# Kernel tuning notes

Hardware: AMD Instinct MI355X
Metric: run time of the kernel (lower is better)

## Reference

```python
import jax, jax.numpy as jnp
import numpy as np

X_DIM = 362
N_EXPERTS = 3
HIDDEN = [1024, 2048, 2048, 1024]  # layer widths; final layer maps back to X_DIM


def _init_params(key):
    dims = [X_DIM] + HIDDEN + [X_DIM]
    params = {}
    for li in range(len(dims) - 1):
        fan_in = dims[li]
        kW, kb, key = jax.random.split(key, 3)
        bound = 1.0 / np.sqrt(fan_in)
        # stacked over experts: [E, in, out]
        params[f"W{li}"] = jax.random.uniform(kW, (N_EXPERTS, dims[li], dims[li + 1]), jnp.float32, -bound, bound)
        params[f"b{li}"] = jax.random.uniform(kb, (N_EXPERTS, dims[li + 1]), jnp.float32, -bound, bound)
    return params


def setup_inputs() -> dict:
    key = jax.random.key(0)
    kx, kn, ka, kp = jax.random.split(key, 4)
    B = 8192
    inp = {
        "batch_x": jax.random.normal(kx, (B, X_DIM), jnp.float32),
        "batch_next": jax.random.normal(kn, (B, X_DIM), jnp.float32),
        "batch_a": jax.random.randint(ka, (B,), 0, N_EXPERTS, jnp.int64),
    }
    inp.update(_init_params(kp))
    return inp


def _experts_forward(x, W0, b0, W1, b1, W2, b2, W3, b3, W4, b4):
    # Run every expert on the full batch (dense grouped GEMMs), then select.
    # h: [E, B, d]
    h = jax.nn.relu(jnp.einsum("bi,eio->ebo", x, W0) + b0[:, None, :])
    h = jax.nn.relu(jnp.einsum("ebi,eio->ebo", h, W1) + b1[:, None, :])
    h = jax.nn.relu(jnp.einsum("ebi,eio->ebo", h, W2) + b2[:, None, :])
    h = jax.nn.relu(jnp.einsum("ebi,eio->ebo", h, W3) + b3[:, None, :])
    return jnp.einsum("ebi,eio->ebo", h, W4) + b4[:, None, :]  # [E, B, X_DIM]


def reference(batch_x, batch_next, batch_a, W0, b0, W1, b1, W2, b2, W3, b3, W4, b4):
    preds = _experts_forward(batch_x, W0, b0, W1, b1, W2, b2, W3, b3, W4, b4)
    # route: pick each sample's prediction from its action's expert
    pred_next = preds[batch_a, jnp.arange(batch_x.shape[0])]  # [B, X_DIM]
    return jnp.mean((pred_next - batch_next) ** 2)
```

## Files before the change

kernel.cpp:

```cpp
#include <hip/hip_runtime.h>
#include <hip/hip_bf16.h>

#define B_SZ   8192
#define XD     362
#define NEXP   3
#define NTILES 70
#define MP     (NTILES*128)

typedef __bf16 bf16x8 __attribute__((ext_vector_type(8)));
typedef float  f32x4  __attribute__((ext_vector_type(4)));

__device__ __forceinline__ unsigned short f2bf(float f) {
    unsigned u = __float_as_uint(f);
    u += 0x7fffu + ((u >> 16) & 1u);
    return (unsigned short)(u >> 16);
}

__global__ __launch_bounds__(1024) void k_route(const int* __restrict__ a,
                                                int* __restrict__ hdr,
                                                int* __restrict__ row_of) {
    __shared__ int sc[3][1024];
    int tid = threadIdx.x;
    int ev[8];
    int c0 = 0, c1 = 0, c2 = 0;
#pragma unroll
    for (int j = 0; j < 8; ++j) {
        int e = a[tid * 8 + j];
        ev[j] = e;
        c0 += (e == 0); c1 += (e == 1); c2 += (e == 2);
    }
    sc[0][tid] = c0; sc[1][tid] = c1; sc[2][tid] = c2;
    __syncthreads();
    for (int off = 1; off < 1024; off <<= 1) {
        int v0 = (tid >= off) ? sc[0][tid - off] : 0;
        int v1 = (tid >= off) ? sc[1][tid - off] : 0;
        int v2 = (tid >= off) ? sc[2][tid - off] : 0;
        __syncthreads();
        sc[0][tid] += v0; sc[1][tid] += v1; sc[2][tid] += v2;
        __syncthreads();
    }
    int tot0 = sc[0][1023], tot1 = sc[1][1023], tot2 = sc[2][1023];
    int t0 = ((tot0 + 255) >> 8) << 1;
    int t1 = ((tot1 + 255) >> 8) << 1;
    int t2 = ((tot2 + 255) >> 8) << 1;
    int seg0 = 0, seg1 = t0 * 128, seg2 = (t0 + t1) * 128;
    int nt = t0 + t1 + t2;
    int b0 = seg0 + sc[0][tid] - c0;
    int b1 = seg1 + sc[1][tid] - c1;
    int b2 = seg2 + sc[2][tid] - c2;
#pragma unroll
    for (int j = 0; j < 8; ++j) {
        int e = ev[j];
        int pos = (e == 0) ? b0++ : (e == 1) ? b1++ : b2++;
        row_of[pos] = tid * 8 + j;
    }
    if (tid == 0) {
        hdr[0] = tot0; hdr[1] = tot1; hdr[2] = tot2;
        hdr[6] = seg0; hdr[7] = seg1; hdr[8] = seg2;
        hdr[12] = nt;
        hdr[13] = nt / 2 - 1;
        hdr[16] = 0;
    }
    if (tid < NTILES)
        hdr[32 + tid] = (tid < t0) ? 0 : (tid < t0 + t1) ? 1 : (tid < nt) ? 2 : -1;
    for (int r = tid; r < MP; r += 1024) {
        int pad;
        if (r < seg1)           pad = (r - seg0) >= tot0;
        else if (r < seg2)      pad = (r - seg1) >= tot1;
        else if (r < nt * 128)  pad = (r - seg2) >= tot2;
        else                    pad = 1;
        if (pad) row_of[r] = -1;
    }
}

__global__ void k_gather(const float* __restrict__ x, const int* __restrict__ row_of,
                         unsigned short* __restrict__ xg) {
    int r = blockIdx.x;
    int c = threadIdx.x;
    int orig = row_of[r];
    float v = (orig >= 0 && c < XD) ? x[(size_t)orig * XD + c] : 0.f;
    xg[(size_t)r * 384 + c] = f2bf(v);
}

__global__ void k_transpose(const float* __restrict__ W, unsigned short* __restrict__ Wt,
                            int K, int N, int Kp, int Np) {
    __shared__ float t[64][33];
    int e  = blockIdx.z;
    int kb = blockIdx.x * 64, nb = blockIdx.y * 32;
    const float* We = W + (size_t)e * K * N;
    unsigned short* Wte = Wt + (size_t)e * Np * Kp;
    int tx = threadIdx.x, ty = threadIdx.y;
#pragma unroll
    for (int j = 0; j < 8; ++j) {
        int k = kb + ty + j * 8, n = nb + tx;
        t[ty + j * 8][tx] = (k < K && n < N) ? We[(size_t)k * N + n] : 0.f;
    }
    __syncthreads();
#pragma unroll
    for (int j = 0; j < 4; ++j) {
        int n = ty + j * 8;
        unsigned int lo = f2bf(t[2 * tx][n]);
        unsigned int hi = f2bf(t[2 * tx + 1][n]);
        *(unsigned int*)&Wte[(size_t)(nb + n) * Kp + kb + 2 * tx] = lo | (hi << 16);
    }
}

template <int TM, int TN, int WAVES, bool FINAL, bool TAIL, bool SKIPLAST>
__global__ __launch_bounds__(WAVES * 64) void k_gemm(
    const unsigned short* __restrict__ A, int lda,
    const unsigned short* __restrict__ Bt, int K, int Np,
    const float* __restrict__ bias, int nvalid,
    unsigned short* __restrict__ C, int ldc,
    const int* __restrict__ hdr,
    const float* __restrict__ nextv, const int* __restrict__ row_of,
    float* __restrict__ accum)
{
    __shared__ unsigned short As[2][TM * 64];
    __shared__ unsigned short Bs[2][TN * 64];
    __shared__ float red[WAVES];

    constexpr int WGN = TN / 64;
    constexpr int LA  = TM / (WAVES * 8);
    constexpr int LB  = TN / (WAVES * 8);

    int mt128;
    if constexpr (TAIL) {
        mt128 = hdr[13] * 2 + blockIdx.y;
    } else {
        if (SKIPLAST && (int)blockIdx.y >= hdr[13] && TM == 256) return;
        mt128 = blockIdx.y * (TM / 128);
    }
    int e = hdr[32 + mt128];
    if (e < 0) return;
    int row0 = mt128 * 128;
    int n0   = blockIdx.x * TN;

    int tid  = threadIdx.x;
    int wid  = tid >> 6, lane = tid & 63;
    int quad = lane >> 4, l15 = lane & 15;
    int sw   = l15 & 7;
    int wm = (wid / WGN) * 64, wn = (wid % WGN) * 64;

    const unsigned short* Ag = A  + (size_t)row0 * lda;
    const unsigned short* Bg = Bt + (size_t)e * Np * K + (size_t)n0 * K;
    const float* be = bias + (size_t)e * nvalid;

    int srow = lane >> 3;
    int scol = ((lane & 7) ^ srow) * 8;

    f32x4 acc[4][4];
#pragma unroll
    for (int i = 0; i < 4; ++i)
#pragma unroll
        for (int j = 0; j < 4; ++j)
            acc[i][j] = (f32x4){0.f, 0.f, 0.f, 0.f};

#define STAGE(K0, P)                                                              \
    {                                                                             \
        _Pragma("unroll")                                                         \
        for (int ii = 0; ii < LA; ++ii) {                                         \
            int rbase = wid * (TM / WAVES) + ii * 8;                              \
            const unsigned short* gp = Ag + (size_t)(rbase + srow) * lda + (K0) + scol; \
            __builtin_amdgcn_global_load_lds(                                     \
                (const __attribute__((address_space(1))) void*)gp,                \
                (__attribute__((address_space(3))) void*)(As[P] + rbase * 64), 16, 0, 0); \
        }                                                                         \
        _Pragma("unroll")                                                         \
        for (int ii = 0; ii < LB; ++ii) {                                         \
            int rbase = wid * (TN / WAVES) + ii * 8;                              \
            const unsigned short* gp = Bg + (size_t)(rbase + srow) * K + (K0) + scol;   \
            __builtin_amdgcn_global_load_lds(                                     \
                (const __attribute__((address_space(1))) void*)gp,                \
                (__attribute__((address_space(3))) void*)(Bs[P] + rbase * 64), 16, 0, 0); \
        }                                                                         \
    }

#define COMPUTE(P)                                                                \
    {                                                                             \
        _Pragma("unroll")                                                         \
        for (int kh = 0; kh < 2; ++kh) {                                          \
            bf16x8 af[4], bfr[4];                                                 \
            _Pragma("unroll")                                                     \
            for (int f = 0; f < 4; ++f) {                                         \
                int row = wm + f * 16 + l15;                                      \
                af[f] = *(const bf16x8*)(As[P] + row * 64 + (((kh * 4 + quad) ^ sw) << 3)); \
            }                                                                     \
            _Pragma("unroll")                                                     \
            for (int f = 0; f < 4; ++f) {                                         \
                int row = wn + f * 16 + l15;                                      \
                bfr[f] = *(const bf16x8*)(Bs[P] + row * 64 + (((kh * 4 + quad) ^ sw) << 3)); \
            }                                                                     \
            _Pragma("unroll")                                                     \
            for (int fm = 0; fm < 4; ++fm)                                        \
                _Pragma("unroll")                                                 \
                for (int fn = 0; fn < 4; ++fn)                                    \
                    acc[fm][fn] = __builtin_amdgcn_mfma_f32_16x16x32_bf16(        \
                        af[fm], bfr[fn], acc[fm][fn], 0, 0, 0);                   \
        }                                                                         \
    }

    STAGE(0, 0);
    __syncthreads();
    for (int k0 = 0; k0 < K; k0 += 128) {
        if (k0 + 64 < K) STAGE(k0 + 64, 1);
        COMPUTE(0);
        __syncthreads();
        if (k0 + 128 < K) STAGE(k0 + 128, 0);
        COMPUTE(1);
        __syncthreads();
    }
#undef STAGE
#undef COMPUTE

    if constexpr (!FINAL) {
#pragma unroll
        for (int fn = 0; fn < 4; ++fn) {
            int n = n0 + wn + fn * 16 + l15;
            float bv = be[n];
#pragma unroll
            for (int fm = 0; fm < 4; ++fm) {
#pragma unroll
                for (int i = 0; i < 4; ++i) {
                    int r = row0 + wm + fm * 16 + quad * 4 + i;
                    float v = acc[fm][fn][i] + bv;
                    v = v > 0.f ? v : 0.f;
                    C[(size_t)r * ldc + n] = f2bf(v);
                }
            }
        }
    } else {
        float local = 0.f;
#pragma unroll
        for (int fm = 0; fm < 4; ++fm) {
#pragma unroll
            for (int i = 0; i < 4; ++i) {
                int r = row0 + wm + fm * 16 + quad * 4 + i;
                int orig = row_of[r];
                if (orig >= 0) {
                    const float* nrow = nextv + (size_t)orig * XD;
#pragma unroll
                    for (int fn = 0; fn < 4; ++fn) {
                        int n = n0 + wn + fn * 16 + l15;
                        if (n < XD) {
                            float v = acc[fm][fn][i] + be[n];
                            float d = v - nrow[n];
                            local += d * d;
                        }
                    }
                }
            }
        }
        for (int off = 32; off > 0; off >>= 1)
            local += __shfl_down(local, off, 64);
        if (lane == 0) red[wid] = local;
        __syncthreads();
        if (tid == 0) {
            float s = 0.f;
#pragma unroll
            for (int w = 0; w < WAVES; ++w) s += red[w];
            atomicAdd(accum, s);
        }
    }
}

__global__ void k_final(const int* hdr, float* out) {
    if (blockIdx.x == 0 && threadIdx.x == 0) {
        float s = ((const float*)hdr)[16];
        out[0] = s / (float)(B_SZ * XD);
    }
}

extern "C" void kernel_launch(void* const* d_in, const int* in_sizes, int n_in,
                              void* d_out, int out_size, void* d_ws, size_t ws_size,
                              hipStream_t stream) {
    const float* x     = (const float*)d_in[0];
    const float* nextv = (const float*)d_in[1];
    const int*   a     = (const int*)d_in[2];
    const float* W0 = (const float*)d_in[3],  *b0 = (const float*)d_in[4];
    const float* W1 = (const float*)d_in[5],  *b1 = (const float*)d_in[6];
    const float* W2 = (const float*)d_in[7],  *b2 = (const float*)d_in[8];
    const float* W3 = (const float*)d_in[9],  *b3 = (const float*)d_in[10];
    const float* W4 = (const float*)d_in[11], *b4 = (const float*)d_in[12];

    int* hdr    = (int*)d_ws;
    int* row_of = hdr + 128;
    unsigned short* xg = (unsigned short*)(row_of + MP);
    unsigned short* hA = xg + (size_t)MP * 384;
    unsigned short* hB = hA + (size_t)MP * 2048;
    unsigned short* Wt = hB + (size_t)MP * 2048;
    float* accum = (float*)(hdr + 16);

    k_route <<<1, 1024, 0, stream>>>(a, hdr, row_of);
    k_gather<<<MP, 384, 0, stream>>>(x, row_of, xg);

    k_transpose<<<dim3(6, 32, 3), dim3(32, 8), 0, stream>>>(W0, Wt, XD, 1024, 384, 1024);
    k_gemm<128, 128, 4, false, false, false><<<dim3(8, NTILES), 256, 0, stream>>>(
        xg, 384, Wt, 384, 1024, b0, 1024, hA, 1024, hdr, nullptr, nullptr, nullptr);

    k_transpose<<<dim3(16, 64, 3), dim3(32, 8), 0, stream>>>(W1, Wt, 1024, 2048, 1024, 2048);
    k_gemm<256, 256, 16, false, false, true><<<dim3(8, NTILES / 2), 1024, 0, stream>>>(
        hA, 1024, Wt, 1024, 2048, b1, 2048, hB, 2048, hdr, nullptr, nullptr, nullptr);
    k_gemm<128, 128, 4, false, true, false><<<dim3(16, 2), 256, 0, stream>>>(
        hA, 1024, Wt, 1024, 2048, b1, 2048, hB, 2048, hdr, nullptr, nullptr, nullptr);

    k_transpose<<<dim3(32, 64, 3), dim3(32, 8), 0, stream>>>(W2, Wt, 2048, 2048, 2048, 2048);
    k_gemm<256, 256, 16, false, false, true><<<dim3(8, NTILES / 2), 1024, 0, stream>>>(
        hB, 2048, Wt, 2048, 2048, b2, 2048, hA, 2048, hdr, nullptr, nullptr, nullptr);
    k_gemm<128, 128, 4, false, true, false><<<dim3(16, 2), 256, 0, stream>>>(
        hB, 2048, Wt, 2048, 2048, b2, 2048, hA, 2048, hdr, nullptr, nullptr, nullptr);

    k_transpose<<<dim3(32, 32, 3), dim3(32, 8), 0, stream>>>(W3, Wt, 2048, 1024, 2048, 1024);
    k_gemm<256, 256, 16, false, false, true><<<dim3(4, NTILES / 2), 1024, 0, stream>>>(
        hA, 2048, Wt, 2048, 1024, b3, 1024, hB, 1024, hdr, nullptr, nullptr, nullptr);
    k_gemm<128, 128, 4, false, true, false><<<dim3(8, 2), 256, 0, stream>>>(
        hA, 2048, Wt, 2048, 1024, b3, 1024, hB, 1024, hdr, nullptr, nullptr, nullptr);

    k_transpose<<<dim3(16, 12, 3), dim3(32, 8), 0, stream>>>(W4, Wt, 1024, XD, 1024, 384);
    k_gemm<128, 128, 4, true, false, false><<<dim3(3, NTILES), 256, 0, stream>>>(
        hB, 1024, Wt, 1024, 384, b4, XD, nullptr, 0, hdr, nextv, row_of, accum);

    k_final<<<1, 64, 0, stream>>>(hdr, (float*)d_out);
}
```

Before: 523.9 us.

## Add 8-wave 256x256 GEMM with global-to-LDS loads and interleaved pipeline

```diff
diff --git a/kernel.cpp b/kernel.cpp
--- a/kernel.cpp
+++ b/kernel.cpp
@@ -263,6 +263,174 @@
     }
 }
 
+template <bool SKIPLAST>
+__global__ __launch_bounds__(512, 2) void k_gemm8(
+    const unsigned short* __restrict__ A, int lda,
+    const unsigned short* __restrict__ Bt, int K, int Np,
+    const float* __restrict__ bias,
+    unsigned short* __restrict__ C, int ldc,
+    const int* __restrict__ hdr)
+{
+    __shared__ unsigned short As[2][256 * 64];
+    __shared__ unsigned short Bs[2][256 * 64];
+
+    if (SKIPLAST && (int)blockIdx.y >= hdr[13]) return;
+    int mt128 = blockIdx.y * 2;
+    int e = hdr[32 + mt128];
+    if (e < 0) return;
+    int row0 = mt128 * 128;
+    int n0   = blockIdx.x * 256;
+
+    int tid  = threadIdx.x;
+    int wid  = tid >> 6, lane = tid & 63;
+    int quad = lane >> 4, l15 = lane & 15;
+    int wmi  = wid >> 2, wni = wid & 3;
+    int srow = lane >> 3;
+    int scol = ((lane & 7) ^ srow) * 8;
+
+    const unsigned short* Ag = A  + (size_t)row0 * lda;
+    const unsigned short* Bg = Bt + (size_t)e * Np * K + (size_t)n0 * K;
+
+    f32x4 acc[8][4];
+#pragma unroll
+    for (int i = 0; i < 8; ++i)
+#pragma unroll
+        for (int j = 0; j < 4; ++j)
+            acc[i][j] = (f32x4){0.f, 0.f, 0.f, 0.f};
+
+    bf16x8 bfr[4][2];
+    bf16x8 af[2][2];
+
+#define STG(GP, LD, DS, H, KC)                                                    \
+    {                                                                             \
+        _Pragma("unroll")                                                         \
+        for (int ii = 0; ii < 2; ++ii) {                                          \
+            int rbase = (H) * 128 + wid * 16 + ii * 8;                            \
+            const unsigned short* gp = (GP) + (size_t)(rbase + srow) * (LD) + (KC) + scol; \
+            __builtin_amdgcn_global_load_lds(                                     \
+                (const __attribute__((address_space(1))) void*)gp,                \
+                (__attribute__((address_space(3))) void*)((DS) + rbase * 64), 16, 0, 0); \
+        }                                                                         \
+    }
+
+#define LDB8(BUF)                                                                 \
+    {                                                                             \
+        _Pragma("unroll")                                                         \
+        for (int nf = 0; nf < 4; ++nf) {                                          \
+            int row = wni * 64 + nf * 16 + l15;                                   \
+            _Pragma("unroll")                                                     \
+            for (int ks = 0; ks < 2; ++ks)                                        \
+                bfr[nf][ks] = *(const bf16x8*)(Bs[BUF] + row * 64 +               \
+                                               (((ks * 4 + quad) ^ (l15 & 7)) << 3)); \
+        }                                                                         \
+    }
+
+#define LDAQ(BUF, Q)                                                              \
+    {                                                                             \
+        _Pragma("unroll")                                                         \
+        for (int mf = 0; mf < 2; ++mf) {                                          \
+            int row = wmi * 128 + ((Q) * 2 + mf) * 16 + l15;                      \
+            _Pragma("unroll")                                                     \
+            for (int ks = 0; ks < 2; ++ks)                                        \
+                af[mf][ks] = *(const bf16x8*)(As[BUF] + row * 64 +                \
+                                              (((ks * 4 + quad) ^ (l15 & 7)) << 3)); \
+        }                                                                         \
+    }
+
+#define MM16(Q)                                                                   \
+    {                                                                             \
+        _Pragma("unroll")                                                         \
+        for (int mf = 0; mf < 2; ++mf)                                            \
+            _Pragma("unroll")                                                     \
+            for (int nf = 0; nf < 4; ++nf)                                        \
+                _Pragma("unroll")                                                 \
+                for (int ks = 0; ks < 2; ++ks)                                    \
+                    acc[(Q) * 2 + mf][nf] = __builtin_amdgcn_mfma_f32_16x16x32_bf16( \
+                        af[mf][ks], bfr[nf][ks], acc[(Q) * 2 + mf][nf], 0, 0, 0); \
+    }
+
+#define BAR    __builtin_amdgcn_s_barrier()
+#define FENCE  asm volatile("" ::: "memory")
+#define LGKM0  { asm volatile("s_waitcnt lgkmcnt(0)" ::: "memory"); __builtin_amdgcn_sched_barrier(0); }
+#define VM4    asm volatile("s_waitcnt vmcnt(4)" ::: "memory")
+#define VM0    asm volatile("s_waitcnt vmcnt(0)" ::: "memory")
+#define PRIO1  __builtin_amdgcn_s_setprio(1)
+#define PRIO0  __builtin_amdgcn_s_setprio(0)
+
+    STG(Ag, lda, As[0], 0, 0);  STG(Ag, lda, As[0], 1, 0);
+    STG(Bg, K,   Bs[0], 0, 0);  STG(Bg, K,   Bs[0], 1, 0);
+    STG(Bg, K,   Bs[1], 0, 64); STG(Bg, K,   Bs[1], 1, 64);
+    VM4; BAR; FENCE;
+
+    int NT = K >> 6;
+    for (int t = 0; t + 4 <= NT; t += 2) {
+        int kc1 = (t + 1) << 6, kc2 = (t + 2) << 6, kc3 = (t + 3) << 6;
+        LDB8(0); LDAQ(0, 0); STG(Ag, lda, As[1], 0, kc1);
+        BAR; LGKM0; PRIO1; MM16(0); PRIO0; BAR; FENCE;
+        LDAQ(0, 1); STG(Ag, lda, As[1], 1, kc1);
+        BAR; LGKM0; PRIO1; MM16(1); PRIO0; BAR; FENCE;
+        LDAQ(0, 2); STG(Bg, K, Bs[0], 0, kc2);
+        BAR; LGKM0; PRIO1; MM16(2); PRIO0; BAR; FENCE;
+        LDAQ(0, 3); STG(Bg, K, Bs[0], 1, kc2);
+        BAR; LGKM0; PRIO1; MM16(3); PRIO0; VM4; BAR; FENCE;
+        LDB8(1); LDAQ(1, 0); STG(Ag, lda, As[0], 0, kc2);
+        BAR; LGKM0; PRIO1; MM16(0); PRIO0; BAR; FENCE;
+        LDAQ(1, 1); STG(Ag, lda, As[0], 1, kc2);
+        BAR; LGKM0; PRIO1; MM16(1); PRIO0; BAR; FENCE;
+        LDAQ(1, 2); STG(Bg, K, Bs[1], 0, kc3);
+        BAR; LGKM0; PRIO1; MM16(2); PRIO0; BAR; FENCE;
+        LDAQ(1, 3); STG(Bg, K, Bs[1], 1, kc3);
+        BAR; LGKM0; PRIO1; MM16(3); PRIO0; VM4; BAR; FENCE;
+    }
+    {
+        int kc1 = (NT - 1) << 6;
+        LDB8(0); LDAQ(0, 0); STG(Ag, lda, As[1], 0, kc1);
+        BAR; LGKM0; PRIO1; MM16(0); PRIO0; BAR; FENCE;
+        LDAQ(0, 1); STG(Ag, lda, As[1], 1, kc1);
+        BAR; LGKM0; PRIO1; MM16(1); PRIO0; BAR; FENCE;
+        LDAQ(0, 2);
+        BAR; LGKM0; PRIO1; MM16(2); PRIO0; BAR; FENCE;
+        LDAQ(0, 3);
+        BAR; LGKM0; PRIO1; MM16(3); PRIO0; VM0; BAR; FENCE;
+        LDB8(1); LDAQ(1, 0);
+        BAR; LGKM0; PRIO1; MM16(0); PRIO0; BAR; FENCE;
+        LDAQ(1, 1);
+        BAR; LGKM0; PRIO1; MM16(1); PRIO0; BAR; FENCE;
+        LDAQ(1, 2);
+        BAR; LGKM0; PRIO1; MM16(2); PRIO0; BAR; FENCE;
+        LDAQ(1, 3);
+        BAR; LGKM0; PRIO1; MM16(3); PRIO0;
+    }
+#undef STG
+#undef LDB8
+#undef LDAQ
+#undef MM16
+#undef BAR
+#undef FENCE
+#undef LGKM0
+#undef VM4
+#undef VM0
+#undef PRIO1
+#undef PRIO0
+
+    const float* be = bias + (size_t)e * Np;
+#pragma unroll
+    for (int nf = 0; nf < 4; ++nf) {
+        int n = n0 + wni * 64 + nf * 16 + l15;
+        float bv = be[n];
+#pragma unroll
+        for (int m8 = 0; m8 < 8; ++m8) {
+#pragma unroll
+            for (int i = 0; i < 4; ++i) {
+                int r = row0 + wmi * 128 + m8 * 16 + quad * 4 + i;
+                float v = acc[m8][nf][i] + bv;
+                v = v > 0.f ? v : 0.f;
+                C[(size_t)r * ldc + n] = f2bf(v);
+            }
+        }
+    }
+}
+
 __global__ void k_final(const int* hdr, float* out) {
     if (blockIdx.x == 0 && threadIdx.x == 0) {
         float s = ((const float*)hdr)[16];
@@ -298,21 +466,19 @@
         xg, 384, Wt, 384, 1024, b0, 1024, hA, 1024, hdr, nullptr, nullptr, nullptr);
 
     k_transpose<<<dim3(16, 64, 3), dim3(32, 8), 0, stream>>>(W1, Wt, 1024, 2048, 1024, 2048);
-    k_gemm<256, 256, 16, false, false, true><<<dim3(8, NTILES / 2), 1024, 0, stream>>>(
-        hA, 1024, Wt, 1024, 2048, b1, 2048, hB, 2048, hdr, nullptr, nullptr, nullptr);
+    k_gemm8<true><<<dim3(8, NTILES / 2), 512, 0, stream>>>(
+        hA, 1024, Wt, 1024, 2048, b1, hB, 2048, hdr);
     k_gemm<128, 128, 4, false, true, false><<<dim3(16, 2), 256, 0, stream>>>(
         hA, 1024, Wt, 1024, 2048, b1, 2048, hB, 2048, hdr, nullptr, nullptr, nullptr);
 
     k_transpose<<<dim3(32, 64, 3), dim3(32, 8), 0, stream>>>(W2, Wt, 2048, 2048, 2048, 2048);
-    k_gemm<256, 256, 16, false, false, true><<<dim3(8, NTILES / 2), 1024, 0, stream>>>(
-        hB, 2048, Wt, 2048, 2048, b2, 2048, hA, 2048, hdr, nullptr, nullptr, nullptr);
+    k_gemm8<true><<<dim3(8, NTILES / 2), 512, 0, stream>>>(
+        hB, 2048, Wt, 2048, 2048, b2, hA, 2048, hdr);
     k_gemm<128, 128, 4, false, true, false><<<dim3(16, 2), 256, 0, stream>>>(
         hB, 2048, Wt, 2048, 2048, b2, 2048, hA, 2048, hdr, nullptr, nullptr, nullptr);
 
     k_transpose<<<dim3(32, 32, 3), dim3(32, 8), 0, stream>>>(W3, Wt, 2048, 1024, 2048, 1024);
-    k_gemm<256, 256, 16, false, false, true><<<dim3(4, NTILES / 2), 1024, 0, stream>>>(
-        hA, 2048, Wt, 2048, 1024, b3, 1024, hB, 1024, hdr, nullptr, nullptr, nullptr);
-    k_gemm<128, 128, 4, false, true, false><<<dim3(8, 2), 256, 0, stream>>>(
+    k_gemm<128, 256, 8, false, false, false><<<dim3(4, NTILES), 512, 0, stream>>>(
         hA, 2048, Wt, 2048, 1024, b3, 1024, hB, 1024, hdr, nullptr, nullptr, nullptr);
 
     k_transpose<<<dim3(16, 12, 3), dim3(32, 8), 0, stream>>>(W4, Wt, 1024, XD, 1024, 384);
```

Measured after the change: 561.4 us. 1.07x slower.
